# Kernel optimization log

Measured on AMD Instinct MI355X. Metric: run time of the kernel, lower is better.

Reference implementation:

```python
import jax, jax.numpy as jnp
import numpy as np

# QP per sample: minimize c^T x + L2_REG * ||x||^2  s.t.  A x = b, lb <= x <= ub
# Solved with ADMM (splitting x = z, z in box), which is the differentiable-through-
# unrolling analogue of the SCS conic solve in the original CvxpyLayer.
L2_REG = 0.1   # config['l2_reg']
RHO = 1.0      # ADMM penalty
N_ITERS = 100  # fixed unrolled iteration count (config['diff_solver_iters'] scaled down)
JITTER = 1e-5

B, M_DIM, N_DIM = 32768, 16, 32


def setup_inputs() -> dict:
    key = jax.random.key(0)
    kA, kx, kc, kl, ku = jax.random.split(key, 5)
    A = jax.random.normal(kA, (B, M_DIM, N_DIM), jnp.float32) / np.sqrt(N_DIM)
    # feasible anchor point so the QP always has a solution
    x0 = jax.random.uniform(kx, (B, N_DIM), jnp.float32, -1.0, 1.0)
    b = jnp.einsum('bmn,bn->bm', A, x0)
    c = jax.random.normal(kc, (B, N_DIM), jnp.float32)
    lb = x0 - jax.random.uniform(kl, (B, N_DIM), jnp.float32, 0.5, 1.5)
    ub = x0 + jax.random.uniform(ku, (B, N_DIM), jnp.float32, 0.5, 1.5)
    return {"A": A, "b": b, "c": c, "lb": lb, "ub": ub}


def _solve_qp(A, b, c, lb, ub):
    sigma = 2.0 * L2_REG + RHO  # Hessian of x-subproblem is sigma*I
    m = A.shape[-2]
    # Gram matrix A A^T, inverted once per sample (small: m x m)
    M = jnp.einsum('bmn,bkn->bmk', A, A) + JITTER * jnp.eye(m, dtype=A.dtype)
    Minv = jnp.linalg.inv(M)

    def step(state, _):
        x, z, u = state
        v = RHO * (z - u) - c
        # equality-constrained x-update via KKT: x = (v - A^T nu)/sigma with A x = b
        rhs = jnp.einsum('bmn,bn->bm', A, v) - sigma * b
        nu = jnp.einsum('bmk,bk->bm', Minv, rhs)
        x = (v - jnp.einsum('bmn,bm->bn', A, nu)) / sigma
        z = jnp.clip(x + u, lb, ub)
        u = u + x - z
        return (x, z, u), None

    z0 = jnp.clip(jnp.zeros_like(c), lb, ub)
    init = (jnp.zeros_like(c), z0, jnp.zeros_like(c))
    (x, z, u), _ = jax.lax.scan(step, init, None, length=N_ITERS)
    return x


def reference(A, b, c, lb, ub):
    return _solve_qp(A, b, c, lb, ub)
```

## Files before the change

### kernel.cpp

```cpp
#include <hip/hip_runtime.h>

typedef float f16v __attribute__((ext_vector_type(16)));
typedef float f4 __attribute__((ext_vector_type(4)));
typedef float f2 __attribute__((ext_vector_type(2)));

template<int I> struct ic { static constexpr int v = I; };
template<int... I> struct iseq {};
template<int N, int... I> struct mk : mk<N-1, N-1, I...> {};
template<int... I> struct mk<0, I...> { using t = iseq<I...>; };
template<class F, int... I>
__device__ __forceinline__ void sfor_impl(F f, iseq<I...>) { (f(ic<I>{}), ...); }
template<int N, class F>
__device__ __forceinline__ void sfor(F f) { sfor_impl(f, typename mk<N>::t{}); }

namespace {
constexpr float kSigma  = 1.2f;
constexpr float kJitter = 1e-5f;
constexpr int   kIters  = 100;
constexpr int   MD = 16;
constexpr int   ND = 32;
constexpr int   SPA = 8;
constexpr int   AS  = 132;
constexpr int   MIS = 20;
constexpr int   MSS = 324;
}

__device__ __forceinline__ float4 lds_a4(const float* As, int r, int j) {
    return *reinterpret_cast<const float4*>(&As[r * 32 + ((j ^ (r & 7)) << 2)]);
}
__device__ __forceinline__ f2 lds_a2(const float* As, int r, int n) {
    return *reinterpret_cast<const f2*>(
        &As[r * 32 + ((((n >> 2) ^ (r & 7)) << 2) | (n & 3))]);
}

__global__ void __launch_bounds__(128)
admm_fused_kernel(const float* __restrict__ Ag, const float* __restrict__ bg,
                  const float* __restrict__ cg, const float* __restrict__ lbg,
                  const float* __restrict__ ubg, float* __restrict__ outg)
{
    __shared__ __align__(16) float A_lds[SPA * AS * 4];
    __shared__ __align__(16) float Mi_lds[SPA * MSS];

    const int t = threadIdx.x;

    {
        const float4* src = reinterpret_cast<const float4*>(Ag) +
                            (size_t)blockIdx.x * (SPA * MD * ND / 4);
        float4* dst = reinterpret_cast<float4*>(A_lds);
        #pragma unroll
        for (int r = 0; r < 8; ++r) {
            int idx = r * 128 + t;
            int smp = idx >> 7;
            int row = (idx >> 3) & 15;
            int j   = idx & 7;
            dst[smp * AS + row * 8 + (j ^ (row & 7))] = src[idx];
        }
    }
    __syncthreads();

    const int lane = t & 63;
    const int l    = lane & 15;
    const int n0   = 2 * l;
    const int smp  = (t >> 6) * 4 + (lane >> 4);
    const size_t gs = (size_t)blockIdx.x * SPA + smp;
    const float* As = &A_lds[smp * AS * 4];
    float* Mi = &Mi_lds[smp * MSS];

    f16v Ar0, Ar1;
    sfor<4>([&](auto J) {
        constexpr int j = decltype(J)::v;
        float4 v  = lds_a4(As, l, j);
        Ar0[4*j+0] = v.x;  Ar0[4*j+1] = v.y;  Ar0[4*j+2] = v.z;  Ar0[4*j+3] = v.w;
        float4 w4 = lds_a4(As, l, j + 4);
        Ar1[4*j+0] = w4.x; Ar1[4*j+1] = w4.y; Ar1[4*j+2] = w4.z; Ar1[4*j+3] = w4.w;
    });

    f16v Mrow, Vrow;
    sfor<16>([&](auto K) {
        constexpr int k = decltype(K)::v;
        float a0 = 0.f, a1 = 0.f, a2 = 0.f, a3 = 0.f;
        sfor<4>([&](auto J) {
            constexpr int j = decltype(J)::v;
            float4 v  = lds_a4(As, k, j);
            a0 += Ar0[4*j+0]*v.x;  a1 += Ar0[4*j+1]*v.y;
            a2 += Ar0[4*j+2]*v.z;  a3 += Ar0[4*j+3]*v.w;
            float4 w4 = lds_a4(As, k, j + 4);
            a0 += Ar1[4*j+0]*w4.x; a1 += Ar1[4*j+1]*w4.y;
            a2 += Ar1[4*j+2]*w4.z; a3 += Ar1[4*j+3]*w4.w;
        });
        Mrow[k] = (a0+a1)+(a2+a3) + ((k == l) ? kJitter : 0.f);
        Vrow[k] = (k == l) ? 1.f : 0.f;
    });

    sfor<16>([&](auto K) {
        constexpr int k = decltype(K)::v;
        float ip = 1.f / __shfl(Mrow[k], k, 16);
        float f  = (l == k) ? 0.f : Mrow[k] * ip;
        sfor<16>([&](auto J) {
            constexpr int j = decltype(J)::v;
            if constexpr (j > k) {
                float mj = __shfl(Mrow[j], k, 16);
                Mrow[j] = (l == k) ? mj * ip : Mrow[j] - f * mj;
            }
        });
        sfor<16>([&](auto J) {
            constexpr int j = decltype(J)::v;
            if constexpr (j < k) {
                float vj = __shfl(Vrow[j], k, 16);
                Vrow[j] = (l == k) ? vj * ip : Vrow[j] - f * vj;
            }
        });
        Vrow[k] = (l == k) ? ip : -f;
    });

    float w = 0.f;
    {
        float bval = bg[gs * MD + l];
        sfor<16>([&](auto K) {
            constexpr int k = decltype(K)::v;
            w += Vrow[k] * __shfl(bval, k, 16);
        });
    }

    sfor<4>([&](auto J) {
        constexpr int j = decltype(J)::v;
        *reinterpret_cast<float4*>(&Mi[l * MIS + 4*j]) =
            make_float4(Vrow[4*j+0], Vrow[4*j+1], Vrow[4*j+2], Vrow[4*j+3]);
    });
    asm volatile("s_waitcnt lgkmcnt(0)" ::: "memory");

    f16v Ca = (f16v)0.0f, Cb = (f16v)0.0f;
    float q0 = 0.f, q1 = 0.f;
    sfor<16>([&](auto K) {
        constexpr int k = decltype(K)::v;
        f2 ak = lds_a2(As, k, n0);
        float wm = __shfl(w, k, 16);
        q0 += ak[0] * wm;
        q1 += ak[1] * wm;
        sfor<4>([&](auto J) {
            constexpr int j = decltype(J)::v;
            float4 mv = *reinterpret_cast<const float4*>(&Mi[k * MIS + 4*j]);
            Ca[4*j+0] += ak[0]*mv.x; Ca[4*j+1] += ak[0]*mv.y;
            Ca[4*j+2] += ak[0]*mv.z; Ca[4*j+3] += ak[0]*mv.w;
            Cb[4*j+0] += ak[1]*mv.x; Cb[4*j+1] += ak[1]*mv.y;
            Cb[4*j+2] += ak[1]*mv.z; Cb[4*j+3] += ak[1]*mv.w;
        });
    });

    f16v P0a = (f16v)0.0f, P0b = (f16v)0.0f;
    f16v P1a = (f16v)0.0f, P1b = (f16v)0.0f;
    sfor<16>([&](auto M) {
        constexpr int m = decltype(M)::v;
        float c0 = Ca[m], c1 = Cb[m];
        sfor<4>([&](auto J) {
            constexpr int j = decltype(J)::v;
            float4 v  = lds_a4(As, m, j);
            P0a[4*j+0] += c0*v.x;  P0a[4*j+1] += c0*v.y;
            P0a[4*j+2] += c0*v.z;  P0a[4*j+3] += c0*v.w;
            P1a[4*j+0] += c1*v.x;  P1a[4*j+1] += c1*v.y;
            P1a[4*j+2] += c1*v.z;  P1a[4*j+3] += c1*v.w;
            float4 w4 = lds_a4(As, m, j + 4);
            P0b[4*j+0] += c0*w4.x; P0b[4*j+1] += c0*w4.y;
            P0b[4*j+2] += c0*w4.z; P0b[4*j+3] += c0*w4.w;
            P1b[4*j+0] += c1*w4.x; P1b[4*j+1] += c1*w4.y;
            P1b[4*j+2] += c1*w4.z; P1b[4*j+3] += c1*w4.w;
        });
    });
    constexpr float is = 1.f / kSigma;
    sfor<16>([&](auto N) {
        constexpr int n = decltype(N)::v;
        P0a[n] = (((n      == n0    ) ? 1.f : 0.f) - P0a[n]) * is;
        P0b[n] = (((n + 16 == n0    ) ? 1.f : 0.f) - P0b[n]) * is;
        P1a[n] = (((n      == n0 + 1) ? 1.f : 0.f) - P1a[n]) * is;
        P1b[n] = (((n + 16 == n0 + 1) ? 1.f : 0.f) - P1b[n]) * is;
    });

    float d0, d1;
    {
        float cv0 = cg[gs * ND + l];
        float cv1 = cg[gs * ND + 16 + l];
        float pc0 = 0.f, pc1 = 0.f;
        sfor<16>([&](auto N) {
            constexpr int n = decltype(N)::v;
            float cn = __shfl(cv0, n, 16);
            pc0 += P0a[n] * cn;
            pc1 += P1a[n] * cn;
        });
        sfor<16>([&](auto N) {
            constexpr int n = decltype(N)::v;
            float cn = __shfl(cv1, n, 16);
            pc0 += P0b[n] * cn;
            pc1 += P1b[n] * cn;
        });
        d0 = q0 - pc0;
        d1 = q1 - pc1;
    }

    f2 lbv = *reinterpret_cast<const f2*>(lbg + gs * ND + n0);
    f2 ubv = *reinterpret_cast<const f2*>(ubg + gs * ND + n0);
    float lb0 = lbv[0], lb1 = lbv[1], ub0 = ubv[0], ub1 = ubv[1];
    float z0 = fminf(fmaxf(0.f, lb0), ub0);
    float z1 = fminf(fmaxf(0.f, lb1), ub1);
    float u0 = 0.f, u1 = 0.f, x0 = 0.f, x1 = 0.f;

    float* Sb = Mi;
    const f4* Sv = reinterpret_cast<const f4*>(Sb);
    for (int it = 0; it < kIters; ++it) {
        f2 sp; sp[0] = z0 - u0; sp[1] = z1 - u1;
        *reinterpret_cast<f2*>(&Sb[n0]) = sp;
        asm volatile("s_waitcnt lgkmcnt(0)" ::: "memory");
        float a0 = 0.f, a1 = 0.f, b0 = 0.f, b1 = 0.f;
        sfor<8>([&](auto Q) {
            constexpr int q = decltype(Q)::v;
            f4 S4 = Sv[q];
            if constexpr (q < 4) {
                constexpr int c = 4 * q;
                a0 = fmaf(P0a[c+0], S4[0], a0); a0 = fmaf(P0a[c+1], S4[1], a0);
                a1 = fmaf(P0a[c+2], S4[2], a1); a1 = fmaf(P0a[c+3], S4[3], a1);
                b0 = fmaf(P1a[c+0], S4[0], b0); b0 = fmaf(P1a[c+1], S4[1], b0);
                b1 = fmaf(P1a[c+2], S4[2], b1); b1 = fmaf(P1a[c+3], S4[3], b1);
            } else {
                constexpr int c = 4 * (q - 4);
                a0 = fmaf(P0b[c+0], S4[0], a0); a0 = fmaf(P0b[c+1], S4[1], a0);
                a1 = fmaf(P0b[c+2], S4[2], a1); a1 = fmaf(P0b[c+3], S4[3], a1);
                b0 = fmaf(P1b[c+0], S4[0], b0); b0 = fmaf(P1b[c+1], S4[1], b0);
                b1 = fmaf(P1b[c+2], S4[2], b1); b1 = fmaf(P1b[c+3], S4[3], b1);
            }
        });
        x0 = d0 + (a0 + a1);
        x1 = d1 + (b0 + b1);
        float t0 = x0 + u0, t1 = x1 + u1;
        z0 = fminf(fmaxf(t0, lb0), ub0);
        z1 = fminf(fmaxf(t1, lb1), ub1);
        u0 = t0 - z0;
        u1 = t1 - z1;
    }

    f2 xo; xo[0] = x0; xo[1] = x1;
    *reinterpret_cast<f2*>(outg + gs * ND + n0) = xo;
}

extern "C" void kernel_launch(void* const* d_in, const int* in_sizes, int n_in,
                              void* d_out, int out_size, void* d_ws, size_t ws_size,
                              hipStream_t stream) {
    const float* A  = (const float*)d_in[0];
    const float* b  = (const float*)d_in[1];
    const float* c  = (const float*)d_in[2];
    const float* lb = (const float*)d_in[3];
    const float* ub = (const float*)d_in[4];
    float* out = (float*)d_out;
    const int B = in_sizes[1] / MD;
    admm_fused_kernel<<<B / SPA, 128, 0, stream>>>(A, b, c, lb, ub, out);
}
```

Baseline: 176.5 us.

## Replace LDS-broadcast matvec in ADMM loop with DPP row-rotate FMAs

The precomputed projection matrix is now stored in a diagonal (rotated) layout per lane, so the per-iteration 32x32 matvec can use v_fmac_f32_dpp with row_ror to pull neighbouring lanes' s values instead of writing s to LDS, waiting, and reading it back. This removes the LDS store/wait/loads from each of the 100 iterations and cuts the held matrix registers from 64 to 64 split differently. The setup is rebuilt so the projector entries are computed directly in the rotated layout, and the c-projection uses matching shuffles. It relies on inline asm DPP semantics within 16-lane rows, and there is a risk of wrong lane mapping or compiler hazards around the DPP instructions.

```diff
diff --git a/kernel.cpp b/kernel.cpp
--- a/kernel.cpp
+++ b/kernel.cpp
@@ -147,51 +147,44 @@
         });
     });
 
-    f16v P0a = (f16v)0.0f, P0b = (f16v)0.0f;
-    f16v P1a = (f16v)0.0f, P1b = (f16v)0.0f;
-    sfor<16>([&](auto M) {
-        constexpr int m = decltype(M)::v;
-        float c0 = Ca[m], c1 = Cb[m];
-        sfor<4>([&](auto J) {
-            constexpr int j = decltype(J)::v;
-            float4 v  = lds_a4(As, m, j);
-            P0a[4*j+0] += c0*v.x;  P0a[4*j+1] += c0*v.y;
-            P0a[4*j+2] += c0*v.z;  P0a[4*j+3] += c0*v.w;
-            P1a[4*j+0] += c1*v.x;  P1a[4*j+1] += c1*v.y;
-            P1a[4*j+2] += c1*v.z;  P1a[4*j+3] += c1*v.w;
-            float4 w4 = lds_a4(As, m, j + 4);
-            P0b[4*j+0] += c0*w4.x; P0b[4*j+1] += c0*w4.y;
-            P0b[4*j+2] += c0*w4.z; P0b[4*j+3] += c0*w4.w;
-            P1b[4*j+0] += c1*w4.x; P1b[4*j+1] += c1*w4.y;
-            P1b[4*j+2] += c1*w4.z; P1b[4*j+3] += c1*w4.w;
-        });
-    });
     constexpr float is = 1.f / kSigma;
-    sfor<16>([&](auto N) {
-        constexpr int n = decltype(N)::v;
-        P0a[n] = (((n      == n0    ) ? 1.f : 0.f) - P0a[n]) * is;
-        P0b[n] = (((n + 16 == n0    ) ? 1.f : 0.f) - P0b[n]) * is;
-        P1a[n] = (((n      == n0 + 1) ? 1.f : 0.f) - P1a[n]) * is;
-        P1b[n] = (((n + 16 == n0 + 1) ? 1.f : 0.f) - P1b[n]) * is;
-    });
+#define QBUILD(j)                                                             \
+    f2 Qa##j, Qb##j;                                                          \
+    {                                                                         \
+        const int n = 2 * ((l - (j)) & 15);                                   \
+        float qa0 = 0.f, qa1 = 0.f, qb0 = 0.f, qb1 = 0.f;                     \
+        sfor<16>([&](auto M) {                                                \
+            constexpr int m = decltype(M)::v;                                 \
+            f2 ak = lds_a2(As, m, n);                                         \
+            qa0 = fmaf(Ca[m], ak[0], qa0); qa1 = fmaf(Ca[m], ak[1], qa1);     \
+            qb0 = fmaf(Cb[m], ak[0], qb0); qb1 = fmaf(Cb[m], ak[1], qb1);     \
+        });                                                                   \
+        Qa##j[0] = ((((j) == 0) ? 1.f : 0.f) - qa0) * is;                     \
+        Qa##j[1] = (0.f - qa1) * is;                                          \
+        Qb##j[0] = (0.f - qb0) * is;                                          \
+        Qb##j[1] = ((((j) == 0) ? 1.f : 0.f) - qb1) * is;                     \
+    }
+    QBUILD(0)  QBUILD(1)  QBUILD(2)  QBUILD(3)
+    QBUILD(4)  QBUILD(5)  QBUILD(6)  QBUILD(7)
+    QBUILD(8)  QBUILD(9)  QBUILD(10) QBUILD(11)
+    QBUILD(12) QBUILD(13) QBUILD(14) QBUILD(15)
+#undef QBUILD
 
     float d0, d1;
     {
-        float cv0 = cg[gs * ND + l];
-        float cv1 = cg[gs * ND + 16 + l];
+        f2 cpr = *reinterpret_cast<const f2*>(cg + gs * ND + n0);
         float pc0 = 0.f, pc1 = 0.f;
-        sfor<16>([&](auto N) {
-            constexpr int n = decltype(N)::v;
-            float cn = __shfl(cv0, n, 16);
-            pc0 += P0a[n] * cn;
-            pc1 += P1a[n] * cn;
-        });
-        sfor<16>([&](auto N) {
-            constexpr int n = decltype(N)::v;
-            float cn = __shfl(cv1, n, 16);
-            pc0 += P0b[n] * cn;
-            pc1 += P1b[n] * cn;
-        });
+#define DSTEP(j) {                                                            \
+        const int cp = (l - (j)) & 15;                                        \
+        float c0 = __shfl(cpr[0], cp, 16);                                    \
+        float c1 = __shfl(cpr[1], cp, 16);                                    \
+        pc0 += Qa##j[0]*c0 + Qa##j[1]*c1;                                     \
+        pc1 += Qb##j[0]*c0 + Qb##j[1]*c1; }
+        DSTEP(0)  DSTEP(1)  DSTEP(2)  DSTEP(3)
+        DSTEP(4)  DSTEP(5)  DSTEP(6)  DSTEP(7)
+        DSTEP(8)  DSTEP(9)  DSTEP(10) DSTEP(11)
+        DSTEP(12) DSTEP(13) DSTEP(14) DSTEP(15)
+#undef DSTEP
         d0 = q0 - pc0;
         d1 = q1 - pc1;
     }
@@ -203,38 +196,33 @@
     float z1 = fminf(fmaxf(0.f, lb1), ub1);
     float u0 = 0.f, u1 = 0.f, x0 = 0.f, x1 = 0.f;
 
-    float* Sb = Mi;
-    const f4* Sv = reinterpret_cast<const f4*>(Sb);
+#define FSTEP(j)                                                              \
+    asm("v_fmac_f32_dpp %0, %1, %2 row_ror:" #j " row_mask:0xf bank_mask:0xf" \
+        : "+v"(ae) : "v"(s0), "v"(Qa##j[0]));                                 \
+    asm("v_fmac_f32_dpp %0, %1, %2 row_ror:" #j " row_mask:0xf bank_mask:0xf" \
+        : "+v"(ao) : "v"(s1), "v"(Qa##j[1]));                                 \
+    asm("v_fmac_f32_dpp %0, %1, %2 row_ror:" #j " row_mask:0xf bank_mask:0xf" \
+        : "+v"(be) : "v"(s0), "v"(Qb##j[0]));                                 \
+    asm("v_fmac_f32_dpp %0, %1, %2 row_ror:" #j " row_mask:0xf bank_mask:0xf" \
+        : "+v"(bo) : "v"(s1), "v"(Qb##j[1]));
+
     for (int it = 0; it < kIters; ++it) {
-        f2 sp; sp[0] = z0 - u0; sp[1] = z1 - u1;
-        *reinterpret_cast<f2*>(&Sb[n0]) = sp;
-        asm volatile("s_waitcnt lgkmcnt(0)" ::: "memory");
-        float a0 = 0.f, a1 = 0.f, b0 = 0.f, b1 = 0.f;
-        sfor<8>([&](auto Q) {
-            constexpr int q = decltype(Q)::v;
-            f4 S4 = Sv[q];
-            if constexpr (q < 4) {
-                constexpr int c = 4 * q;
-                a0 = fmaf(P0a[c+0], S4[0], a0); a0 = fmaf(P0a[c+1], S4[1], a0);
-                a1 = fmaf(P0a[c+2], S4[2], a1); a1 = fmaf(P0a[c+3], S4[3], a1);
-                b0 = fmaf(P1a[c+0], S4[0], b0); b0 = fmaf(P1a[c+1], S4[1], b0);
-                b1 = fmaf(P1a[c+2], S4[2], b1); b1 = fmaf(P1a[c+3], S4[3], b1);
-            } else {
-                constexpr int c = 4 * (q - 4);
-                a0 = fmaf(P0b[c+0], S4[0], a0); a0 = fmaf(P0b[c+1], S4[1], a0);
-                a1 = fmaf(P0b[c+2], S4[2], a1); a1 = fmaf(P0b[c+3], S4[3], a1);
-                b0 = fmaf(P1b[c+0], S4[0], b0); b0 = fmaf(P1b[c+1], S4[1], b0);
-                b1 = fmaf(P1b[c+2], S4[2], b1); b1 = fmaf(P1b[c+3], S4[3], b1);
-            }
-        });
-        x0 = d0 + (a0 + a1);
-        x1 = d1 + (b0 + b1);
+        float s0 = z0 - u0, s1 = z1 - u1;
+        float ae = d0, ao = 0.f, be = d1, bo = 0.f;
+        ae = fmaf(Qa0[0], s0, ae); ao = fmaf(Qa0[1], s1, ao);
+        be = fmaf(Qb0[0], s0, be); bo = fmaf(Qb0[1], s1, bo);
+        FSTEP(1)  FSTEP(2)  FSTEP(3)  FSTEP(4)  FSTEP(5)
+        FSTEP(6)  FSTEP(7)  FSTEP(8)  FSTEP(9)  FSTEP(10)
+        FSTEP(11) FSTEP(12) FSTEP(13) FSTEP(14) FSTEP(15)
+        x0 = ae + ao;
+        x1 = be + bo;
         float t0 = x0 + u0, t1 = x1 + u1;
         z0 = fminf(fmaxf(t0, lb0), ub0);
         z1 = fminf(fmaxf(t1, lb1), ub1);
         u0 = t0 - z0;
         u1 = t1 - z1;
     }
+#undef FSTEP
 
     f2 xo; xo[0] = x0; xo[1] = x1;
     *reinterpret_cast<f2*>(outg + gs * ND + n0) = xo;
```

Result: faster. 170.2 us (-3.6%).
